# Kernel optimization log

Hardware: AMD Instinct MI355X
Metric: run time of the kernel (lower is better)

The kernel has to match this reference:

```python
import jax, jax.numpy as jnp
import numpy as np


def setup_inputs() -> dict:
    key = jax.random.key(0)
    ks = jax.random.split(key, 6)
    B, d, S = 256, 512, 196  # batch, hidden dim, spatial locations (14x14)
    return {
        "memory_state": jax.random.normal(ks[0], (B, d), dtype=jnp.float32),
        "ctrl_state": jax.random.normal(ks[1], (B, d), dtype=jnp.float32),
        "kb_proj": jax.random.normal(ks[2], (B, d, S), dtype=jnp.float32),
        "W_concat": jax.random.normal(ks[3], (d, d), dtype=jnp.float32) * (1.0 / np.sqrt(d)),
        "b_concat": jax.random.normal(ks[4], (d,), dtype=jnp.float32) * 0.01,
        "w_attn": jax.random.normal(ks[5], (d,), dtype=jnp.float32) * (1.0 / np.sqrt(d)),
    }


def reference(memory_state, ctrl_state, kb_proj, W_concat, b_concat, w_attn):
    # I_elements: [B, S, d] -- elementwise gating of knowledge base by memory
    I_t = memory_state[:, :, None] * kb_proj           # [B, d, S]
    I_t = jnp.transpose(I_t, (0, 2, 1))                # [B, S, d]
    # concat_layer (torch Linear: x @ W^T + b) + residual with kb_proj
    concat = jnp.einsum('bsd,ed->bse', I_t, W_concat) + b_concat
    concat = concat + jnp.transpose(kb_proj, (0, 2, 1))  # [B, S, d]
    # attention logits: (concat * ctrl) @ w_attn -> [B, S]
    rai = jnp.einsum('bsd,d->bs', concat * ctrl_state[:, None, :], w_attn)
    rvi = jax.nn.softmax(rai, axis=1)                  # [B, S]
    # attention-weighted sum over spatial locations -> [B, d]
    read_vector = jnp.einsum('bs,bds->bd', rvi, kb_proj)
    return read_vector
```

## Files before the change

kernel.cpp:

```cpp
#include <hip/hip_runtime.h>
#include <math.h>

#define B 256
#define D 512
#define S 196
#define SQ 49
#define NCH 8
#define CH 64


__global__ __launch_bounds__(256) void k_gemm_part(const float* __restrict__ ctrl,
                                                   const float* __restrict__ w_attn,
                                                   const float* __restrict__ W,
                                                   float* __restrict__ gpart) {
    __shared__ float u_s[CH];
    const int bid = blockIdx.x;
    const int b = bid >> 3, c = bid & 7;
    const int t = threadIdx.x;
    if (t < CH) {
        const int e = c * CH + t;
        u_s[t] = ctrl[b * D + e] * w_attn[e];
    }
    __syncthreads();
    float a0 = 0.f, a1 = 0.f;
    for (int i = 0; i < CH; ++i) {
        const int e = c * CH + i;
        a0 += u_s[i] * W[e * D + t];
        a1 += u_s[i] * W[e * D + t + 256];
    }
    gpart[(size_t)bid * D + t]       = a0;
    gpart[(size_t)bid * D + t + 256] = a1;
}

__global__ __launch_bounds__(256) void k_prep2(const float* __restrict__ gpart,
                                               const float* __restrict__ mem,
                                               const float* __restrict__ ctrl,
                                               const float* __restrict__ w_attn,
                                               float* __restrict__ p) {
    const int idx = blockIdx.x * 256 + threadIdx.x;
    const int d = idx & 511;
    float s = 0.f;
#pragma unroll
    for (int c = 0; c < NCH; ++c)
        s += gpart[((size_t)(idx >> 9) * NCH + c) * D + d];
    p[idx] = mem[idx] * s + ctrl[idx] * w_attn[d];
}

__global__ __launch_bounds__(256) void k_logits(const float* __restrict__ kb,
                                                const float* __restrict__ p,
                                                float* __restrict__ rai_part) {
    __shared__ float p_s[CH];
    __shared__ float part[4][S];
    const int bid = blockIdx.x;
    const int b = bid >> 3, c = bid & 7;
    const int t = threadIdx.x;
    const int w = t >> 6, l = t & 63;
    if (t < CH) p_s[t] = p[b * D + c * CH + t];
    __syncthreads();
    const float* base = kb + (size_t)b * D * S + (size_t)c * CH * S;
    if (l < SQ) {
        float4 acc = {0.f, 0.f, 0.f, 0.f};
        for (int i = 0; i < 16; ++i) {
            const int r = w * 16 + i;
            const float4 v = *(const float4*)(base + (size_t)r * S + 4 * l);
            const float pv = p_s[r];
            acc.x += pv * v.x; acc.y += pv * v.y;
            acc.z += pv * v.z; acc.w += pv * v.w;
        }
        *(float4*)&part[w][4 * l] = acc;
    }
    __syncthreads();
    if (t < S)
        rai_part[(size_t)bid * S + t] = (part[0][t] + part[1][t]) + (part[2][t] + part[3][t]);
}

__global__ __launch_bounds__(256) void k_softmax(const float* __restrict__ rai_part,
                                                 float* __restrict__ rvi) {
    __shared__ float redm[4], reds[4];
    const int b = blockIdx.x;
    const int t = threadIdx.x, w = t >> 6, l = t & 63;
    float rai = -INFINITY;
    if (t < S) {
        float v = 0.f;
#pragma unroll
        for (int c = 0; c < NCH; ++c)
            v += rai_part[((size_t)b * NCH + c) * S + t];
        rai = v;
    }
    float m = rai;
#pragma unroll
    for (int o = 1; o < 64; o <<= 1) m = fmaxf(m, __shfl_xor(m, o, 64));
    if (l == 0) redm[w] = m;
    __syncthreads();
    m = fmaxf(fmaxf(redm[0], redm[1]), fmaxf(redm[2], redm[3]));
    float ex = (t < S) ? __expf(rai - m) : 0.f;
    float sm = ex;
#pragma unroll
    for (int o = 1; o < 64; o <<= 1) sm += __shfl_xor(sm, o, 64);
    if (l == 0) reds[w] = sm;
    __syncthreads();
    const float li = (reds[0] + reds[1]) + (reds[2] + reds[3]);
    if (t < S) rvi[b * S + t] = ex / li;
}

__global__ __launch_bounds__(256) void k_wsum(const float* __restrict__ kb,
                                              const float* __restrict__ rvi,
                                              float* __restrict__ out) {
    __shared__ float rvi_s[S];
    const int bid = blockIdx.x;
    const int b = bid >> 5, r0 = (bid & 31) * 16;
    const int t = threadIdx.x, w = t >> 6, l = t & 63;
    if (t < S) rvi_s[t] = rvi[b * S + t];
    __syncthreads();
    float4 rv = {0.f, 0.f, 0.f, 0.f};
    if (l < SQ) rv = *(const float4*)&rvi_s[4 * l];
#pragma unroll
    for (int i = 0; i < 4; ++i) {
        const int e = r0 + w * 4 + i;
        float a = 0.f;
        if (l < SQ) {
            const float4 v = *(const float4*)(kb + ((size_t)b * D + e) * S + 4 * l);
            a = rv.x * v.x + rv.y * v.y + rv.z * v.z + rv.w * v.w;
        }
#pragma unroll
        for (int o = 1; o < 64; o <<= 1) a += __shfl_xor(a, o, 64);
        if (l == 0) out[b * D + e] = a;
    }
}

extern "C" void kernel_launch(void* const* d_in, const int* in_sizes, int n_in,
                              void* d_out, int out_size, void* d_ws, size_t ws_size,
                              hipStream_t stream) {
    const float* mem  = (const float*)d_in[0];
    const float* ctrl = (const float*)d_in[1];
    const float* kb   = (const float*)d_in[2];
    const float* W    = (const float*)d_in[3];
    const float* wat  = (const float*)d_in[5];
    float* out = (float*)d_out;

    float* gpart    = (float*)d_ws;
    float* p        = gpart + (size_t)B * NCH * D;
    float* rai_part = p + (size_t)B * D;
    float* rvi      = rai_part + (size_t)B * NCH * S;

    k_gemm_part<<<B * NCH,     256, 0, stream>>>(ctrl, wat, W, gpart);
    k_prep2    <<<B * D / 256, 256, 0, stream>>>(gpart, mem, ctrl, wat, p);
    k_logits   <<<B * NCH,     256, 0, stream>>>(kb, p, rai_part);
    k_softmax  <<<B,           256, 0, stream>>>(rai_part, rvi);
    k_wsum     <<<B * D / 16,  256, 0, stream>>>(kb, rvi, out);
}
```

Measured before the change: 194.3 us.

## Fuse prep into logits, softmax into wsum, and batch GEMM over 8 rows

The GEMM kernel now handles 8 batch rows per block, reusing each loaded W element across 8 batches instead of reloading W once per batch. The prep reduction is folded into the logits kernel and the softmax into the weighted-sum kernel, cutting five launches to three and removing the p and rvi round trips through global memory. In exchange, every wsum block redundantly recomputes the softmax for its batch, and the GEMM grid shrinks to 256 blocks.

```diff
diff --git a/kernel.cpp b/kernel.cpp
--- a/kernel.cpp
+++ b/kernel.cpp
@@ -6,85 +6,113 @@
 #define S 196
 #define SQ 49
 #define NCH 8
-#define CH 64
 
-
-__global__ __launch_bounds__(256) void k_gemm_part(const float* __restrict__ ctrl,
-                                                   const float* __restrict__ w_attn,
-                                                   const float* __restrict__ W,
-                                                   float* __restrict__ gpart) {
-    __shared__ float u_s[CH];
-    const int bid = blockIdx.x;
-    const int b = bid >> 3, c = bid & 7;
+__global__ __launch_bounds__(256) void k_gemm(const float* __restrict__ ctrl,
+                                              const float* __restrict__ w_attn,
+                                              const float* __restrict__ W,
+                                              float* __restrict__ gpart) {
+    __shared__ float u_s[64][8];
+    const int ce = blockIdx.x >> 5;
+    const int b0 = (blockIdx.x & 31) * 8;
     const int t = threadIdx.x;
-    if (t < CH) {
-        const int e = c * CH + t;
-        u_s[t] = ctrl[b * D + e] * w_attn[e];
+#pragma unroll
+    for (int k = t; k < 512; k += 256) {
+        const int j = k & 7, el = k >> 3;
+        const int e = ce * 64 + el;
+        u_s[el][j] = ctrl[(b0 + j) * D + e] * w_attn[e];
     }
     __syncthreads();
-    float a0 = 0.f, a1 = 0.f;
-    for (int i = 0; i < CH; ++i) {
-        const int e = c * CH + i;
-        a0 += u_s[i] * W[e * D + t];
-        a1 += u_s[i] * W[e * D + t + 256];
+    float a0[8], a1[8];
+#pragma unroll
+    for (int j = 0; j < 8; ++j) { a0[j] = 0.f; a1[j] = 0.f; }
+    for (int e0 = 0; e0 < 64; e0 += 4) {
+        float w0[4], w1[4];
+#pragma unroll
+        for (int i = 0; i < 4; ++i) {
+            const int e = ce * 64 + e0 + i;
+            w0[i] = W[e * D + t];
+            w1[i] = W[e * D + t + 256];
+        }
+#pragma unroll
+        for (int i = 0; i < 4; ++i) {
+            const float4 ua = *(const float4*)&u_s[e0 + i][0];
+            const float4 ub = *(const float4*)&u_s[e0 + i][4];
+            a0[0] += ua.x * w0[i]; a0[1] += ua.y * w0[i];
+            a0[2] += ua.z * w0[i]; a0[3] += ua.w * w0[i];
+            a0[4] += ub.x * w0[i]; a0[5] += ub.y * w0[i];
+            a0[6] += ub.z * w0[i]; a0[7] += ub.w * w0[i];
+            a1[0] += ua.x * w1[i]; a1[1] += ua.y * w1[i];
+            a1[2] += ua.z * w1[i]; a1[3] += ua.w * w1[i];
+            a1[4] += ub.x * w1[i]; a1[5] += ub.y * w1[i];
+            a1[6] += ub.z * w1[i]; a1[7] += ub.w * w1[i];
+        }
     }
-    gpart[(size_t)bid * D + t]       = a0;
-    gpart[(size_t)bid * D + t + 256] = a1;
-}
-
-__global__ __launch_bounds__(256) void k_prep2(const float* __restrict__ gpart,
-                                               const float* __restrict__ mem,
-                                               const float* __restrict__ ctrl,
-                                               const float* __restrict__ w_attn,
-                                               float* __restrict__ p) {
-    const int idx = blockIdx.x * 256 + threadIdx.x;
-    const int d = idx & 511;
-    float s = 0.f;
 #pragma unroll
-    for (int c = 0; c < NCH; ++c)
-        s += gpart[((size_t)(idx >> 9) * NCH + c) * D + d];
-    p[idx] = mem[idx] * s + ctrl[idx] * w_attn[d];
+    for (int j = 0; j < 8; ++j) {
+        gpart[((size_t)(b0 + j) * NCH + ce) * D + t]       = a0[j];
+        gpart[((size_t)(b0 + j) * NCH + ce) * D + t + 256] = a1[j];
+    }
 }
 
 __global__ __launch_bounds__(256) void k_logits(const float* __restrict__ kb,
-                                                const float* __restrict__ p,
+                                                const float* __restrict__ gpart,
+                                                const float* __restrict__ mem,
+                                                const float* __restrict__ ctrl,
+                                                const float* __restrict__ w_attn,
                                                 float* __restrict__ rai_part) {
-    __shared__ float p_s[CH];
+    __shared__ float p_s[64];
     __shared__ float part[4][S];
     const int bid = blockIdx.x;
     const int b = bid >> 3, c = bid & 7;
     const int t = threadIdx.x;
     const int w = t >> 6, l = t & 63;
-    if (t < CH) p_s[t] = p[b * D + c * CH + t];
+    if (t < 64) {
+        const int d = c * 64 + t;
+        float s = 0.f;
+#pragma unroll
+        for (int ce = 0; ce < NCH; ++ce)
+            s += gpart[((size_t)b * NCH + ce) * D + d];
+        p_s[t] = mem[b * D + d] * s + ctrl[b * D + d] * w_attn[d];
+    }
     __syncthreads();
-    const float* base = kb + (size_t)b * D * S + (size_t)c * CH * S;
+    const float* base = kb + (size_t)b * D * S + (size_t)c * 64 * S;
     if (l < SQ) {
-        float4 acc = {0.f, 0.f, 0.f, 0.f};
-        for (int i = 0; i < 16; ++i) {
-            const int r = w * 16 + i;
-            const float4 v = *(const float4*)(base + (size_t)r * S + 4 * l);
-            const float pv = p_s[r];
-            acc.x += pv * v.x; acc.y += pv * v.y;
-            acc.z += pv * v.z; acc.w += pv * v.w;
+        float4 acc0 = {0.f, 0.f, 0.f, 0.f}, acc1 = {0.f, 0.f, 0.f, 0.f};
+        for (int i = 0; i < 8; ++i) {
+            const int r0 = w * 16 + i, r1 = w * 16 + 8 + i;
+            const float4 v0 = *(const float4*)(base + (size_t)r0 * S + 4 * l);
+            const float4 v1 = *(const float4*)(base + (size_t)r1 * S + 4 * l);
+            const float pv0 = p_s[r0], pv1 = p_s[r1];
+            acc0.x += pv0 * v0.x; acc0.y += pv0 * v0.y;
+            acc0.z += pv0 * v0.z; acc0.w += pv0 * v0.w;
+            acc1.x += pv1 * v1.x; acc1.y += pv1 * v1.y;
+            acc1.z += pv1 * v1.z; acc1.w += pv1 * v1.w;
         }
-        *(float4*)&part[w][4 * l] = acc;
+        part[w][4 * l + 0] = acc0.x + acc1.x;
+        part[w][4 * l + 1] = acc0.y + acc1.y;
+        part[w][4 * l + 2] = acc0.z + acc1.z;
+        part[w][4 * l + 3] = acc0.w + acc1.w;
     }
     __syncthreads();
     if (t < S)
         rai_part[(size_t)bid * S + t] = (part[0][t] + part[1][t]) + (part[2][t] + part[3][t]);
 }
 
-__global__ __launch_bounds__(256) void k_softmax(const float* __restrict__ rai_part,
-                                                 float* __restrict__ rvi) {
+__global__ __launch_bounds__(256) void k_wsum(const float* __restrict__ kb,
+                                              const float* __restrict__ rai_part,
+                                              float* __restrict__ out) {
+    __shared__ float rvi_s[S];
     __shared__ float redm[4], reds[4];
-    const int b = blockIdx.x;
-    const int t = threadIdx.x, w = t >> 6, l = t & 63;
+    const int bid = blockIdx.x;
+    const int b = bid >> 3, c = bid & 7;
+    const int t = threadIdx.x;
+    const int w = t >> 6, l = t & 63;
     float rai = -INFINITY;
     if (t < S) {
         float v = 0.f;
 #pragma unroll
-        for (int c = 0; c < NCH; ++c)
-            v += rai_part[((size_t)b * NCH + c) * S + t];
+        for (int k = 0; k < NCH; ++k)
+            v += rai_part[((size_t)b * NCH + k) * S + t];
         rai = v;
     }
     float m = rai;
@@ -100,31 +128,31 @@
     if (l == 0) reds[w] = sm;
     __syncthreads();
     const float li = (reds[0] + reds[1]) + (reds[2] + reds[3]);
-    if (t < S) rvi[b * S + t] = ex / li;
-}
+    if (t < S) rvi_s[t] = ex / li;
+    __syncthreads();
 
-__global__ __launch_bounds__(256) void k_wsum(const float* __restrict__ kb,
-                                              const float* __restrict__ rvi,
-                                              float* __restrict__ out) {
-    __shared__ float rvi_s[S];
-    const int bid = blockIdx.x;
-    const int b = bid >> 5, r0 = (bid & 31) * 16;
-    const int t = threadIdx.x, w = t >> 6, l = t & 63;
-    if (t < S) rvi_s[t] = rvi[b * S + t];
-    __syncthreads();
     float4 rv = {0.f, 0.f, 0.f, 0.f};
     if (l < SQ) rv = *(const float4*)&rvi_s[4 * l];
+    const float* base = kb + (size_t)b * D * S + (size_t)c * 64 * S;
 #pragma unroll
-    for (int i = 0; i < 4; ++i) {
-        const int e = r0 + w * 4 + i;
-        float a = 0.f;
+    for (int i = 0; i < 8; ++i) {
+        const int r0 = w * 16 + i, r1 = w * 16 + 8 + i;
+        float a0 = 0.f, a1 = 0.f;
         if (l < SQ) {
-            const float4 v = *(const float4*)(kb + ((size_t)b * D + e) * S + 4 * l);
-            a = rv.x * v.x + rv.y * v.y + rv.z * v.z + rv.w * v.w;
+            const float4 v0 = *(const float4*)(base + (size_t)r0 * S + 4 * l);
+            const float4 v1 = *(const float4*)(base + (size_t)r1 * S + 4 * l);
+            a0 = rv.x * v0.x + rv.y * v0.y + rv.z * v0.z + rv.w * v0.w;
+            a1 = rv.x * v1.x + rv.y * v1.y + rv.z * v1.z + rv.w * v1.w;
         }
 #pragma unroll
-        for (int o = 1; o < 64; o <<= 1) a += __shfl_xor(a, o, 64);
-        if (l == 0) out[b * D + e] = a;
+        for (int o = 1; o < 64; o <<= 1) {
+            a0 += __shfl_xor(a0, o, 64);
+            a1 += __shfl_xor(a1, o, 64);
+        }
+        if (l == 0) {
+            out[(size_t)b * D + c * 64 + r0] = a0;
+            out[(size_t)b * D + c * 64 + r1] = a1;
+        }
     }
 }
 
@@ -139,13 +167,9 @@
     float* out = (float*)d_out;
 
     float* gpart    = (float*)d_ws;
-    float* p        = gpart + (size_t)B * NCH * D;
-    float* rai_part = p + (size_t)B * D;
-    float* rvi      = rai_part + (size_t)B * NCH * S;
+    float* rai_part = gpart + (size_t)B * NCH * D;
 
-    k_gemm_part<<<B * NCH,     256, 0, stream>>>(ctrl, wat, W, gpart);
-    k_prep2    <<<B * D / 256, 256, 0, stream>>>(gpart, mem, ctrl, wat, p);
-    k_logits   <<<B * NCH,     256, 0, stream>>>(kb, p, rai_part);
-    k_softmax  <<<B,           256, 0, stream>>>(rai_part, rvi);
-    k_wsum     <<<B * D / 16,  256, 0, stream>>>(kb, rvi, out);
+    k_gemm  <<<256,     256, 0, stream>>>(ctrl, wat, W, gpart);
+    k_logits<<<B * NCH, 256, 0, stream>>>(kb, gpart, mem, ctrl, wat, rai_part);
+    k_wsum  <<<B * NCH, 256, 0, stream>>>(kb, rai_part, out);
 }
```

Result: faster. 189.6 us (-2.4%).
